# Kernel optimization log

Measured on AMD Instinct MI355X. Metric: run time of the kernel, lower is better.

Reference implementation:

```python
import jax, jax.numpy as jnp
import numpy as np
from jax import lax

TOTAL_LENGTH = 1024
EMBED_DIM = 128
GRAPH_DIM = 50257
N_STEP = 128  # min_len
BATCH = 32


def setup_inputs() -> dict:
    key = jax.random.key(0)
    k1, k2, k3, k4, k5, k6, k7 = jax.random.split(key, 7)
    s_e = 1.0 / np.sqrt(EMBED_DIM)
    return {
        "zi": jax.random.randint(k1, (BATCH,), 0, TOTAL_LENGTH),
        "y": jax.random.randint(k2, (BATCH, N_STEP), 0, GRAPH_DIM),
        "latent": jax.random.normal(k3, (TOTAL_LENGTH, EMBED_DIM), dtype=jnp.float32) * s_e,
        "Wt": jax.random.normal(k4, (EMBED_DIM, EMBED_DIM), dtype=jnp.float32) * s_e,
        "bt": jax.random.normal(k5, (EMBED_DIM,), dtype=jnp.float32) * s_e,
        "Wv": jax.random.normal(k6, (GRAPH_DIM, EMBED_DIM), dtype=jnp.float32) * s_e,
        "bv": jax.random.normal(k7, (GRAPH_DIM,), dtype=jnp.float32) * s_e,
    }


def reference(zi, y, latent, Wt, bt, Wv, bv):
    # z0: [B, E] gathered from latent table
    z0 = latent[zi]

    def step(z, _):
        # emit current z, then update: z <- tanh(z + transition(z))
        z_next = jnp.tanh(z + z @ Wt.T + bt)
        return z_next, z

    _, zs = lax.scan(step, z0, None, length=N_STEP)  # [T, B, E]
    zs = jnp.transpose(zs, (1, 0, 2))                # [B, T, E]
    logits = jnp.einsum("bte,ve->btv", zs, Wv) + bv  # [B, T, V]
    ys = jax.nn.log_softmax(logits, axis=-1)
    yp = jnp.take_along_axis(ys, y[:, :, None], axis=-1)[:, :, 0]  # [B, T]
    return yp
```

## Files before the change

### kernel.cpp

```cpp
#include <hip/hip_runtime.h>
#include <hip/hip_bf16.h>
#include <hip/hip_fp16.h>

#define EMBED 128
#define TSTEPS 128
#define NBATCH 32
#define VDIM 50257
#define VPAD 50304
#define MROWS 4096
#define NGROUPS 786
#define GRIDX 64
#define GRIDY 16
#define MAXGRP 13
#define CONV_N4 ((VDIM * EMBED) / 4)
#define CONV_BLOCKS ((CONV_N4 + 255) / 256)

static constexpr float LOG2E = 1.4426950408889634f;
static constexpr float LN2   = 0.6931471805599453f;

__device__ __forceinline__ float fast_exp2(float x) {
#if __has_builtin(__builtin_amdgcn_exp2f)
    return __builtin_amdgcn_exp2f(x);
#else
    return exp2f(x);
#endif
}
__device__ __forceinline__ float fast_log2(float x) {
#if __has_builtin(__builtin_amdgcn_logf)
    return __builtin_amdgcn_logf(x);
#else
    return log2f(x);
#endif
}
__device__ __forceinline__ unsigned short f2bf_raw(float f) {
    __hip_bfloat16 h = __float2bfloat16(f);
    union { __hip_bfloat16 b; unsigned short u; } cvt;
    cvt.b = h;
    return cvt.u;
}
__device__ __forceinline__ float bf_raw2f(unsigned short u) {
    union { unsigned int u; float f; } cvt;
    cvt.u = ((unsigned int)u) << 16;
    return cvt.f;
}

__global__ __launch_bounds__(256) void setup_kernel(const int* __restrict__ zi,
                                                    const float* __restrict__ latent,
                                                    const float* __restrict__ Wt,
                                                    const float* __restrict__ bt,
                                                    const float* __restrict__ Wv,
                                                    const float* __restrict__ bv,
                                                    unsigned short* __restrict__ zsb,
                                                    unsigned short* __restrict__ Wvb,
                                                    float* __restrict__ bvs,
                                                    float* __restrict__ S) {
    if (blockIdx.x >= NBATCH) {
        const int cb = blockIdx.x - NBATCH;
        if (cb == 0) {
#pragma unroll
            for (int i = 0; i < MROWS / 256; i++)
                S[i * 256 + threadIdx.x] = 0.f;
        }
        if (cb == 1) {
            const int base4 = (VDIM * EMBED) / 4;
            const int npad4 = ((VPAD - VDIM) * EMBED) / 4;
            for (int i = threadIdx.x; i < npad4; i += 256)
                reinterpret_cast<ushort4*>(Wvb)[base4 + i] = make_ushort4(0, 0, 0, 0);
        }
        const int idx = cb * 256 + threadIdx.x;
        if (idx < VPAD)
            bvs[idx] = (idx < VDIM) ? bv[idx] * LOG2E : -1e30f;
        if (idx < CONV_N4) {
            float4 v = reinterpret_cast<const float4*>(Wv)[idx];
            ushort4 o;
            o.x = f2bf_raw(v.x); o.y = f2bf_raw(v.y);
            o.z = f2bf_raw(v.z); o.w = f2bf_raw(v.w);
            reinterpret_cast<ushort4*>(Wvb)[idx] = o;
        }
        return;
    }

    __shared__ float zbuf[2][EMBED];
    const int b = blockIdx.x;
    const int e = threadIdx.x >> 1;
    const int h = threadIdx.x & 1;

    float4 wrow[16];
    const float4* wt4 = reinterpret_cast<const float4*>(Wt + e * EMBED + h * 64);
#pragma unroll
    for (int i = 0; i < 16; i++) wrow[i] = wt4[i];
    const float bte = bt[e];

    if (h == 0) zbuf[0][e] = latent[zi[b] * EMBED + e];
    __syncthreads();

    int cur = 0;
    for (int t = 0; t < TSTEPS; t++) {
        const float zc = zbuf[cur][e];
        const long row = (long)b * TSTEPS + t;
        if (h == 0)
            zsb[row * EMBED + e] = f2bf_raw(zc * LOG2E);

        const float4* z4 = reinterpret_cast<const float4*>(&zbuf[cur][h * 64]);
        float4 acc = {0.f, 0.f, 0.f, 0.f};
#pragma unroll
        for (int i = 0; i < 16; i++) {
            float4 zv = z4[i];
            acc.x += zv.x * wrow[i].x;
            acc.y += zv.y * wrow[i].y;
            acc.z += zv.z * wrow[i].z;
            acc.w += zv.w * wrow[i].w;
        }
        float v = acc.x + acc.y + acc.z + acc.w;
        float p = __shfl_xor(v, 1);
        float sA = h ? p : v;
        float sB = h ? v : p;
        float znew = tanhf(((zc + sA) + sB) + bte);
        if (h == 0) zbuf[cur ^ 1][e] = znew;
        __syncthreads();
        cur ^= 1;
    }
}

typedef __attribute__((ext_vector_type(8))) short bfrag;
typedef __attribute__((ext_vector_type(4))) float f32x4;

__global__ __launch_bounds__(256) void gemm_lse_kernel(const unsigned short* __restrict__ zsb,
                                                       const unsigned short* __restrict__ Wvb,
                                                       const float* __restrict__ bvs,
                                                       float* __restrict__ S) {
    __shared__ short ldsb[2][8192];
    __shared__ float ldsbias[MAXGRP * 64];

    const int lane  = threadIdx.x & 63;
    const int wave  = threadIdx.x >> 6;
    const int col16 = lane & 15;
    const int quad  = lane >> 4;
    const int mbase = blockIdx.y * 256 + wave * 64;

    const int x  = blockIdx.x;
    const int g0 = x * 12 + min(x, 18);
    const int g1 = g0 + 12 + (x < 18 ? 1 : 0);
    const int nbias = (g1 - g0) * 64;

    for (int i = threadIdx.x; i < nbias; i += 256)
        ldsbias[i] = bvs[g0 * 64 + i];

    bfrag a[4][4];
    const short* zss = reinterpret_cast<const short*>(zsb);
#pragma unroll
    for (int s = 0; s < 4; s++)
#pragma unroll
        for (int c = 0; c < 4; c++) {
            const short* p = zss + (long)(mbase + s * 16 + col16) * EMBED + c * 32 + quad * 8;
            a[s][c] = *reinterpret_cast<const bfrag*>(p);
        }

    float sums[16];
#pragma unroll
    for (int i = 0; i < 16; i++) sums[i] = 0.f;

    const short* wvs = reinterpret_cast<const short*>(Wvb);

    auto stage = [&](int buf, int g) {
#pragma unroll
        for (int j = 0; j < 4; j++) {
            const int r   = (wave * 4 + j) * 4 + quad;
            const int swz = col16 ^ (r & 15);
            const short* gp = wvs + (long)(g * 64 + r) * EMBED + swz * 8;
            __builtin_amdgcn_global_load_lds(
                (const __attribute__((address_space(1))) void*)gp,
                (__attribute__((address_space(3))) void*)&ldsb[buf][(wave * 4 + j) * 512],
                16, 0, 0);
        }
    };

    int cur = 0;
    stage(0, g0);

    const f32x4 dzero = {0.f, 0.f, 0.f, 0.f};

    for (int g = g0; g < g1; g++) {
        __syncthreads();
        if (g + 1 < g1) stage(cur ^ 1, g + 1);

        const float* biasg = &ldsbias[(g - g0) * 64];

#pragma unroll
        for (int c = 0; c < 4; c++) {
            bfrag bf[4];
#pragma unroll
            for (int kc = 0; kc < 4; kc++)
                bf[kc] = *reinterpret_cast<const bfrag*>(
                    &ldsb[cur][(c * 16 + col16) * 128 + (((kc * 4 + quad) ^ col16) * 8)]);

            const float eb = fast_exp2(biasg[c * 16 + col16]);

            f32x4 d[4];
#pragma unroll
            for (int s = 0; s < 4; s++)
                d[s] = __builtin_amdgcn_mfma_f32_16x16x32_bf16(a[s][0], bf[0], dzero, 0, 0, 0);
#pragma unroll
            for (int kc = 1; kc < 4; kc++)
#pragma unroll
                for (int s = 0; s < 4; s++)
                    d[s] = __builtin_amdgcn_mfma_f32_16x16x32_bf16(a[s][kc], bf[kc], d[s], 0, 0, 0);

#pragma unroll
            for (int s = 0; s < 4; s++)
#pragma unroll
                for (int r = 0; r < 4; r++)
                    sums[s * 4 + r] = fmaf(fast_exp2(d[s][r]), eb, sums[s * 4 + r]);
        }
        cur ^= 1;
    }

#pragma unroll
    for (int s = 0; s < 4; s++) {
#pragma unroll
        for (int r = 0; r < 4; r++) {
            float v = sums[s * 4 + r];
            v += __shfl_xor(v, 1);
            v += __shfl_xor(v, 2);
            v += __shfl_xor(v, 4);
            v += __shfl_xor(v, 8);
            if (col16 == 0)
                atomicAdd(&S[mbase + s * 16 + quad * 4 + r], v);
        }
    }
}

__global__ __launch_bounds__(256) void tail_kernel(const unsigned short* __restrict__ zsb,
                                                   const float* __restrict__ Wv,
                                                   const float* __restrict__ bv,
                                                   const int* __restrict__ y,
                                                   const float* __restrict__ S,
                                                   float* __restrict__ out) {
    const int row  = blockIdx.x * 4 + (threadIdx.x >> 6);
    const int lane = threadIdx.x & 63;
    const int yv = y[row];
    const ushort2* zr = reinterpret_cast<const ushort2*>(zsb + (long)row * EMBED);
    const float2*  wr = reinterpret_cast<const float2*>(Wv + (long)yv * EMBED);
    ushort2 z2 = zr[lane];
    float2  w2 = wr[lane];
    float v = bf_raw2f(z2.x) * w2.x + bf_raw2f(z2.y) * w2.y;
    v += __shfl_xor(v, 32);
    v += __shfl_xor(v, 16);
    v += __shfl_xor(v, 8);
    v += __shfl_xor(v, 4);
    v += __shfl_xor(v, 2);
    v += __shfl_xor(v, 1);
    if (lane == 0)
        out[row] = LN2 * (v - fast_log2(S[row])) + bv[yv];
}

extern "C" void kernel_launch(void* const* d_in, const int* in_sizes, int n_in,
                              void* d_out, int out_size, void* d_ws, size_t ws_size,
                              hipStream_t stream) {
    const int*   zi     = (const int*)d_in[0];
    const int*   y      = (const int*)d_in[1];
    const float* latent = (const float*)d_in[2];
    const float* Wt     = (const float*)d_in[3];
    const float* bt     = (const float*)d_in[4];
    const float* Wv     = (const float*)d_in[5];
    const float* bv     = (const float*)d_in[6];
    float* out = (float*)d_out;

    char* ws = (char*)d_ws;
    unsigned short* zsb = (unsigned short*)ws;
    float*          S   = (float*)(ws + (1u << 20));
    float*          bvs = (float*)(ws + (1u << 20) + (64u << 10));
    unsigned short* wvb = (unsigned short*)(ws + (2u << 20));

    setup_kernel<<<NBATCH + CONV_BLOCKS, 256, 0, stream>>>(zi, latent, Wt, bt, Wv, bv,
                                                           zsb, wvb, bvs, S);

    gemm_lse_kernel<<<dim3(GRIDX, GRIDY), 256, 0, stream>>>(zsb, wvb, bvs, S);

    tail_kernel<<<MROWS / 4, 256, 0, stream>>>(zsb, Wv, bv, y, S, out);
}
```

Baseline: 214.6 us.

## Double GEMM grid width, precompute exp2 bias, stash recurrent states in LDS

The vocab-chunked GEMM+logsumexp grid is doubled in x (about 6-7 column groups per block instead of 12-13), giving more blocks for the GPU's CUs. The bias is converted to exp2 form once in setup and read straight from global memory, so the per-block LDS bias load and the per-chunk exp2 are gone. The recurrent scan writes bf16 states into a 32KB LDS stash and copies them out with vectorized stores at the end instead of scattered 2-byte global stores. The trade-offs are more atomics on S, a shorter double-buffer pipeline per block, and extra LDS use in the setup blocks.

```diff
diff --git a/kernel.cpp b/kernel.cpp
--- a/kernel.cpp
+++ b/kernel.cpp
@@ -1,6 +1,5 @@
 #include <hip/hip_runtime.h>
 #include <hip/hip_bf16.h>
-#include <hip/hip_fp16.h>
 
 #define EMBED 128
 #define TSTEPS 128
@@ -9,9 +8,8 @@
 #define VPAD 50304
 #define MROWS 4096
 #define NGROUPS 786
-#define GRIDX 64
+#define GRIDX 128
 #define GRIDY 16
-#define MAXGRP 13
 #define CONV_N4 ((VDIM * EMBED) / 4)
 #define CONV_BLOCKS ((CONV_N4 + 255) / 256)
 
@@ -52,7 +50,7 @@
                                                     const float* __restrict__ bv,
                                                     unsigned short* __restrict__ zsb,
                                                     unsigned short* __restrict__ Wvb,
-                                                    float* __restrict__ bvs,
+                                                    float* __restrict__ ebt,
                                                     float* __restrict__ S) {
     if (blockIdx.x >= NBATCH) {
         const int cb = blockIdx.x - NBATCH;
@@ -69,7 +67,7 @@
         }
         const int idx = cb * 256 + threadIdx.x;
         if (idx < VPAD)
-            bvs[idx] = (idx < VDIM) ? bv[idx] * LOG2E : -1e30f;
+            ebt[idx] = (idx < VDIM) ? fast_exp2(bv[idx] * LOG2E) : 0.f;
         if (idx < CONV_N4) {
             float4 v = reinterpret_cast<const float4*>(Wv)[idx];
             ushort4 o;
@@ -81,6 +79,7 @@
     }
 
     __shared__ float zbuf[2][EMBED];
+    __shared__ unsigned short zstash[TSTEPS * EMBED];
     const int b = blockIdx.x;
     const int e = threadIdx.x >> 1;
     const int h = threadIdx.x & 1;
@@ -97,9 +96,8 @@
     int cur = 0;
     for (int t = 0; t < TSTEPS; t++) {
         const float zc = zbuf[cur][e];
-        const long row = (long)b * TSTEPS + t;
         if (h == 0)
-            zsb[row * EMBED + e] = f2bf_raw(zc * LOG2E);
+            zstash[t * EMBED + e] = f2bf_raw(zc * LOG2E);
 
         const float4* z4 = reinterpret_cast<const float4*>(&zbuf[cur][h * 64]);
         float4 acc = {0.f, 0.f, 0.f, 0.f};
@@ -120,6 +118,11 @@
         __syncthreads();
         cur ^= 1;
     }
+
+    uint4* dst = reinterpret_cast<uint4*>(zsb + (long)b * TSTEPS * EMBED);
+    const uint4* src = reinterpret_cast<const uint4*>(zstash);
+    for (int i = threadIdx.x; i < TSTEPS * EMBED / 8; i += 256)
+        dst[i] = src[i];
 }
 
 typedef __attribute__((ext_vector_type(8))) short bfrag;
@@ -127,10 +130,9 @@
 
 __global__ __launch_bounds__(256) void gemm_lse_kernel(const unsigned short* __restrict__ zsb,
                                                        const unsigned short* __restrict__ Wvb,
-                                                       const float* __restrict__ bvs,
+                                                       const float* __restrict__ ebt,
                                                        float* __restrict__ S) {
     __shared__ short ldsb[2][8192];
-    __shared__ float ldsbias[MAXGRP * 64];
 
     const int lane  = threadIdx.x & 63;
     const int wave  = threadIdx.x >> 6;
@@ -139,12 +141,8 @@
     const int mbase = blockIdx.y * 256 + wave * 64;
 
     const int x  = blockIdx.x;
-    const int g0 = x * 12 + min(x, 18);
-    const int g1 = g0 + 12 + (x < 18 ? 1 : 0);
-    const int nbias = (g1 - g0) * 64;
-
-    for (int i = threadIdx.x; i < nbias; i += 256)
-        ldsbias[i] = bvs[g0 * 64 + i];
+    const int g0 = x * 6 + min(x, 18);
+    const int g1 = g0 + 6 + (x < 18 ? 1 : 0);
 
     bfrag a[4][4];
     const short* zss = reinterpret_cast<const short*>(zsb);
@@ -184,7 +182,9 @@
         __syncthreads();
         if (g + 1 < g1) stage(cur ^ 1, g + 1);
 
-        const float* biasg = &ldsbias[(g - g0) * 64];
+        float ebl[4];
+#pragma unroll
+        for (int c = 0; c < 4; c++) ebl[c] = ebt[g * 64 + c * 16 + col16];
 
 #pragma unroll
         for (int c = 0; c < 4; c++) {
@@ -194,8 +194,6 @@
                 bf[kc] = *reinterpret_cast<const bfrag*>(
                     &ldsb[cur][(c * 16 + col16) * 128 + (((kc * 4 + quad) ^ col16) * 8)]);
 
-            const float eb = fast_exp2(biasg[c * 16 + col16]);
-
             f32x4 d[4];
 #pragma unroll
             for (int s = 0; s < 4; s++)
@@ -210,7 +208,7 @@
             for (int s = 0; s < 4; s++)
 #pragma unroll
                 for (int r = 0; r < 4; r++)
-                    sums[s * 4 + r] = fmaf(fast_exp2(d[s][r]), eb, sums[s * 4 + r]);
+                    sums[s * 4 + r] = fmaf(fast_exp2(d[s][r]), ebl[c], sums[s * 4 + r]);
         }
         cur ^= 1;
     }
@@ -269,13 +267,13 @@
     char* ws = (char*)d_ws;
     unsigned short* zsb = (unsigned short*)ws;
     float*          S   = (float*)(ws + (1u << 20));
-    float*          bvs = (float*)(ws + (1u << 20) + (64u << 10));
+    float*          ebt = (float*)(ws + (1u << 20) + (64u << 10));
     unsigned short* wvb = (unsigned short*)(ws + (2u << 20));
 
     setup_kernel<<<NBATCH + CONV_BLOCKS, 256, 0, stream>>>(zi, latent, Wt, bt, Wv, bv,
-                                                           zsb, wvb, bvs, S);
-
-    gemm_lse_kernel<<<dim3(GRIDX, GRIDY), 256, 0, stream>>>(zsb, wvb, bvs, S);
+                                                           zsb, wvb, ebt, S);
+
+    gemm_lse_kernel<<<dim3(GRIDX, GRIDY), 256, 0, stream>>>(zsb, wvb, ebt, S);
 
     tail_kernel<<<MROWS / 4, 256, 0, stream>>>(zsb, Wv, bv, y, S, out);
 }
```

New measurement: 228.3 us. +6.4%, slower.
